# Kernel optimization log

Hardware: AMD Instinct MI355X
Metric: run time of the kernel (lower is better)

The kernel has to match this reference:

```python
import jax, jax.numpy as jnp
import numpy as np
import math

H = 5       # attention heads
DK = 20     # attdim // H
ATT = 100   # attdim
LAYERS = 2
B, L, BERT_DIM = 32, 256, 768


def _layernorm(x, a, b, eps=1e-6):
    mean = x.mean(-1, keepdims=True)
    std = jnp.std(x, axis=-1, ddof=1, keepdims=True)  # torch.std is unbiased
    return a * (x - mean) / (std + eps) + b


def _forward(sequence_output, src_mask, aspect_mask, short_mask,
             ln_a, ln_b, Wxx_w, Wxx_b, q_w, q_b, k_w, k_b,
             dense_w, dense_b, bias_m, W_w, W_b, Wx_w, Wx_b, clf_w, clf_b):
    Bn, Ln, _ = sequence_output.shape
    x = _layernorm(sequence_output, ln_a, ln_b)
    g = x @ Wxx_w + Wxx_b                                  # [B,L,100]
    asp_wn = aspect_mask.sum(1, keepdims=True)             # [B,1]
    aspect = (g * aspect_mask[..., None]).sum(1) / asp_wn  # [B,100]

    q = (g @ q_w + q_b).reshape(Bn, Ln, H, DK).transpose(0, 2, 1, 3)  # [B,H,L,dk]
    k = (g @ k_w + k_b).reshape(Bn, Ln, H, DK).transpose(0, 2, 1, 3)
    # aspect is expanded identically across heads/positions before dense -> [B,dk]
    asp = aspect @ dense_w + dense_b                       # [B,dk]
    scores = jnp.einsum('bhid,bhjd->bhij', q, k) / math.sqrt(DK)
    asp_sc = jnp.tanh(jnp.einsum('bd,bhjd->bhj', asp, k) + bias_m[0])
    scores = scores + asp_sc[:, :, None, :]
    scores = jnp.where(src_mask[:, None, None, :] == 0, -1e9, scores)
    scores = scores + short_mask                           # [B,1,L,L] broadcast
    adj = jax.nn.softmax(scores, axis=-1)                  # [B,H,L,L]

    # edge-update linear split so the [B,L,L,205] concat is never materialized:
    # edge[b,i,j] = adj_perm[b,i,j] @ Wa + go[b,j] @ W1 + go[b,i] @ W2 + b
    Wa, W1, W2 = Wx_w[:H], Wx_w[H:H + ATT], Wx_w[H + ATT:]
    go = g
    for i in range(LAYERS):
        # expand+matmul+mean over heads == mean-head message passing
        Ax = jnp.einsum('bhij,bjd->bid', adj, go) / H
        go = jax.nn.relu(Ax @ W_w + W_b)
        if i < LAYERS - 1:  # last edge update is discarded by the original output
            edge = (jnp.einsum('bhij,hk->bijk', adj, Wa)
                    + (go @ W1)[:, None, :, :]
                    + (go @ W2)[:, :, None, :]
                    + Wx_b)
            adj = edge.transpose(0, 3, 1, 2)
    # original: node_outputs = F.relu(gcn_outputs) (aggregate_W result is overwritten)
    h = jax.nn.relu(go)
    out1 = (h * aspect_mask[..., None]).sum(1) / asp_wn    # [B,100]
    return out1 @ clf_w + clf_b                            # [B,3]


def setup_inputs() -> dict:
    key = jax.random.key(0)
    ks = jax.random.split(key, 24)
    f32 = jnp.float32
    p = lambda k, shape, s=0.05: jax.random.normal(k, shape, dtype=f32) * s
    src_mask = jax.random.randint(ks[0], (B, L), 0, 2, dtype=jnp.int32).at[:, 0].set(1)
    aspect_mask = jnp.zeros((B, L), f32).at[:, 4:8].set(1.0)  # aspect span tokens
    return {
        'sequence_output': jax.random.normal(ks[1], (B, L, BERT_DIM), dtype=f32),
        'src_mask': src_mask,
        'aspect_mask': aspect_mask,
        'short_mask': p(ks[2], (B, 1, L, L), 1.0),
        'ln_a': jnp.ones((BERT_DIM,), f32),
        'ln_b': jnp.zeros((BERT_DIM,), f32),
        'Wxx_w': p(ks[3], (BERT_DIM, ATT)), 'Wxx_b': p(ks[4], (ATT,)),
        'q_w': p(ks[5], (ATT, ATT)), 'q_b': p(ks[6], (ATT,)),
        'k_w': p(ks[7], (ATT, ATT)), 'k_b': p(ks[8], (ATT,)),
        'dense_w': p(ks[9], (ATT, DK)), 'dense_b': p(ks[10], (DK,)),
        'bias_m': p(ks[11], (1,)),
        'W_w': p(ks[12], (ATT, ATT)), 'W_b': p(ks[13], (ATT,)),
        'Wx_w': p(ks[14], (H + 2 * ATT, H)), 'Wx_b': p(ks[15], (H,)),
        'clf_w': p(ks[16], (ATT, 3)), 'clf_b': p(ks[17], (3,)),
    }


def reference(sequence_output, src_mask, aspect_mask, short_mask,
              ln_a, ln_b, Wxx_w, Wxx_b, q_w, q_b, k_w, k_b,
              dense_w, dense_b, bias_m, W_w, W_b, Wx_w, Wx_b, clf_w, clf_b):
    return _forward(sequence_output, src_mask, aspect_mask, short_mask,
                    ln_a, ln_b, Wxx_w, Wxx_b, q_w, q_b, k_w, k_b,
                    dense_w, dense_b, bias_m, W_w, W_b, Wx_w, Wx_b, clf_w, clf_b)
```

## Files before the change

kernel.cpp:

```cpp
#include <hip/hip_runtime.h>
#include <math.h>

constexpr int CL = 256;
constexpr int CD = 768;
constexpr int CATT = 100;
constexpr int CH = 5;
constexpr int CDK = 20;
constexpr unsigned NBLK = 512;

__device__ __forceinline__ void fma4(float4& a, float s, const float4& w) {
    a.x = fmaf(s, w.x, a.x);
    a.y = fmaf(s, w.y, a.y);
    a.z = fmaf(s, w.z, a.z);
    a.w = fmaf(s, w.w, a.w);
}

__device__ __forceinline__ void bbar(unsigned* ctr, unsigned target, bool poll) {
    __syncthreads();
    if (threadIdx.x == 0) {
        __hip_atomic_fetch_add(ctr, 1u, __ATOMIC_RELEASE, __HIP_MEMORY_SCOPE_AGENT);
        if (poll) {
            while (__hip_atomic_load(ctr, __ATOMIC_RELAXED, __HIP_MEMORY_SCOPE_AGENT) < target) {
                __builtin_amdgcn_s_sleep(2);
            }
        }
    }
    __syncthreads();
    __builtin_amdgcn_fence(__ATOMIC_ACQUIRE, "agent");
}

__global__ __launch_bounds__(256, 2) void fused_all(
    const float* __restrict__ x, const int* __restrict__ src_mask,
    const float* __restrict__ amask, const float* __restrict__ shortm,
    const float* __restrict__ ln_a, const float* __restrict__ ln_b,
    const float* __restrict__ Wxx_w, const float* __restrict__ Wxx_b,
    const float* __restrict__ q_w, const float* __restrict__ q_b,
    const float* __restrict__ k_w, const float* __restrict__ k_b,
    const float* __restrict__ dense_w, const float* __restrict__ dense_b,
    const float* __restrict__ bias_m, const float* __restrict__ W_w,
    const float* __restrict__ W_b, const float* __restrict__ Wx_w,
    const float* __restrict__ Wx_b, const float* __restrict__ clf_w,
    const float* __restrict__ clf_b,
    float* __restrict__ g, float* __restrict__ ktb,
    float* __restrict__ go1, float* __restrict__ aspect_raw,
    float* __restrict__ t1, float* __restrict__ t2,
    float* __restrict__ out1_raw, unsigned* __restrict__ bar,
    float* __restrict__ out)
{
    __shared__ __align__(16) float S[12744];

    const int t = threadIdx.x;
    const int lane = t & 63, wid = t >> 6;
    const int blk = blockIdx.x;
    const int xcd = blk & 7;
    const int slot = blk >> 3;
    const int batch = xcd * 4 + (slot >> 4);
    const int icb = slot & 15;
    unsigned* bctr = bar + batch * 32;

    {
        float* s_wB   = S + 4160;
        float* s_xn   = S + 0;
        float* s_gt   = S + 1152;
        float* s_ln   = S + 10560;
        float* s_qq   = S + 10560;
        float* s_mean = S + 12160;
        float* s_rinv = S + 12176;
        const int r0 = batch * 256 + icb * 16;

        if (t < 192) {
            ((float4*)s_ln)[t] = ((const float4*)ln_a)[t];
            ((float4*)(s_ln + 768))[t] = ((const float4*)ln_b)[t];
        }

        for (int rr = wid * 4; rr < wid * 4 + 4; ++rr) {
            const float* xr = x + (size_t)(r0 + rr) * CD;
            float xv[12];
            float s = 0.f;
#pragma unroll
            for (int m = 0; m < 12; ++m) { xv[m] = xr[lane + 64 * m]; s += xv[m]; }
#pragma unroll
            for (int o = 32; o; o >>= 1) s += __shfl_xor(s, o);
            float mean = s * (1.0f / 768.0f);
            float sq = 0.f;
#pragma unroll
            for (int m = 0; m < 12; ++m) { float d = xv[m] - mean; sq = fmaf(d, d, sq); }
#pragma unroll
            for (int o = 32; o; o >>= 1) sq += __shfl_xor(sq, o);
            if (lane == 0) {
                s_mean[rr] = mean;
                s_rinv[rr] = 1.0f / (sqrtf(sq * (1.0f / 767.0f)) + 1e-6f);
            }
        }

        const float4* wsrc = (const float4*)Wxx_w;
        float4 w0 = wsrc[t], w1 = wsrc[t + 256], w2 = wsrc[t + 512], w3;
        if (t < 32) w3 = wsrc[t + 768];
        const int rA = t >> 5, cA = t & 31;
        float xa = x[(size_t)(r0 + rA) * CD + cA];
        float xb = x[(size_t)(r0 + rA + 8) * CD + cA];

        __syncthreads();

        {
            float4* d4 = (float4*)s_wB;
            d4[t] = w0; d4[t + 256] = w1; d4[t + 512] = w2;
            if (t < 32) d4[t + 768] = w3;
            float la = s_ln[cA], lbv = s_ln[768 + cA];
            s_xn[rA * 36 + cA] = fmaf(la, (xa - s_mean[rA]) * s_rinv[rA], lbv);
            s_xn[(rA + 8) * 36 + cA] = fmaf(la, (xb - s_mean[rA + 8]) * s_rinv[rA + 8], lbv);
        }
        __syncthreads();

        const int cgi = t % 25, rg = t / 25;
        const int c = cgi * 4;
        float4 acc0 = make_float4(0.f, 0.f, 0.f, 0.f);
        float4 acc1 = make_float4(0.f, 0.f, 0.f, 0.f);

        for (int kt = 0; kt < 24; ++kt) {
            if (kt < 23) {
                const float4* ws = wsrc + (size_t)(kt + 1) * 800;
                w0 = ws[t]; w1 = ws[t + 256]; w2 = ws[t + 512];
                if (t < 32) w3 = ws[t + 768];
                int gc = (kt + 1) * 32 + cA;
                xa = x[(size_t)(r0 + rA) * CD + gc];
                xb = x[(size_t)(r0 + rA + 8) * CD + gc];
            }
            if (t < 200) {
                const float* wb = s_wB + (kt & 1) * 3200;
                const float* xbuf = s_xn + (kt & 1) * 576;
#pragma unroll 2
                for (int kk = 0; kk < 32; kk += 4) {
                    float4 a0 = *(const float4*)&xbuf[(rg * 2 + 0) * 36 + kk];
                    float4 a1 = *(const float4*)&xbuf[(rg * 2 + 1) * 36 + kk];
                    float4 v0 = *(const float4*)&wb[(kk + 0) * 100 + c];
                    float4 v1 = *(const float4*)&wb[(kk + 1) * 100 + c];
                    float4 v2 = *(const float4*)&wb[(kk + 2) * 100 + c];
                    float4 v3 = *(const float4*)&wb[(kk + 3) * 100 + c];
                    fma4(acc0, a0.x, v0); fma4(acc0, a0.y, v1); fma4(acc0, a0.z, v2); fma4(acc0, a0.w, v3);
                    fma4(acc1, a1.x, v0); fma4(acc1, a1.y, v1); fma4(acc1, a1.z, v2); fma4(acc1, a1.w, v3);
                }
            }
            if (kt < 23) {
                float4* d4 = (float4*)(s_wB + ((kt + 1) & 1) * 3200);
                d4[t] = w0; d4[t + 256] = w1; d4[t + 512] = w2;
                if (t < 32) d4[t + 768] = w3;
                int gc = (kt + 1) * 32 + cA;
                float la = s_ln[gc], lbv = s_ln[768 + gc];
                float* xd = s_xn + ((kt + 1) & 1) * 576;
                xd[rA * 36 + cA] = fmaf(la, (xa - s_mean[rA]) * s_rinv[rA], lbv);
                xd[(rA + 8) * 36 + cA] = fmaf(la, (xb - s_mean[rA + 8]) * s_rinv[rA + 8], lbv);
            }
            __syncthreads();
        }

        if (t < 200) {
            float4 bias = *(const float4*)&Wxx_b[c];
            float4 rv0, rv1;
            rv0.x = acc0.x + bias.x; rv0.y = acc0.y + bias.y; rv0.z = acc0.z + bias.z; rv0.w = acc0.w + bias.w;
            rv1.x = acc1.x + bias.x; rv1.y = acc1.y + bias.y; rv1.z = acc1.z + bias.z; rv1.w = acc1.w + bias.w;
            float4 rv[2] = { rv0, rv1 };
#pragma unroll
            for (int q = 0; q < 2; ++q) {
                int row = r0 + rg * 2 + q;
                *(float4*)&g[(size_t)row * CATT + c] = rv[q];
                *(float4*)&s_gt[(rg * 2 + q) * 100 + c] = rv[q];
                float m = amask[row];
                if (m != 0.f) {
                    atomicAdd(&aspect_raw[batch * CATT + c + 0], m * rv[q].x);
                    atomicAdd(&aspect_raw[batch * CATT + c + 1], m * rv[q].y);
                    atomicAdd(&aspect_raw[batch * CATT + c + 2], m * rv[q].z);
                    atomicAdd(&aspect_raw[batch * CATT + c + 3], m * rv[q].w);
                }
            }
        }

        const float4* qw4 = (const float4*)q_w;
        const float4* kw4 = (const float4*)k_w;
        float4 sA = qw4[t], sB;
        if (t < 244) sB = qw4[t + 256];
        __syncthreads();
        {
            float4* d4 = (float4*)s_wB;
            d4[t] = sA; if (t < 244) d4[t + 256] = sB;
        }
        __syncthreads();

        float4 p0 = make_float4(0.f, 0.f, 0.f, 0.f);
        float4 p1 = make_float4(0.f, 0.f, 0.f, 0.f);
        for (int tau = 0; tau < 10; ++tau) {
            if (tau < 9) {
                const float4* src = (tau + 1 < 5) ? qw4 + (size_t)(tau + 1) * 500
                                                  : kw4 + (size_t)(tau - 4) * 500;
                sA = src[t]; if (t < 244) sB = src[t + 256];
            }
            if (t < 200) {
                const float* wb = s_wB + (tau & 1) * 3200;
                const int kb = (tau % 5) * 20;
#pragma unroll 2
                for (int kk = 0; kk < 20; kk += 4) {
                    float4 a0 = *(const float4*)&s_gt[(rg * 2 + 0) * 100 + kb + kk];
                    float4 a1 = *(const float4*)&s_gt[(rg * 2 + 1) * 100 + kb + kk];
                    float4 v0 = *(const float4*)&wb[(kk + 0) * 100 + c];
                    float4 v1 = *(const float4*)&wb[(kk + 1) * 100 + c];
                    float4 v2 = *(const float4*)&wb[(kk + 2) * 100 + c];
                    float4 v3 = *(const float4*)&wb[(kk + 3) * 100 + c];
                    fma4(p0, a0.x, v0); fma4(p0, a0.y, v1); fma4(p0, a0.z, v2); fma4(p0, a0.w, v3);
                    fma4(p1, a1.x, v0); fma4(p1, a1.y, v1); fma4(p1, a1.z, v2); fma4(p1, a1.w, v3);
                }
                if (tau == 4 || tau == 9) {
                    const float* bb = (tau == 4) ? q_b : k_b;
                    float4 bias = *(const float4*)&bb[c];
                    p0.x += bias.x; p0.y += bias.y; p0.z += bias.z; p0.w += bias.w;
                    p1.x += bias.x; p1.y += bias.y; p1.z += bias.z; p1.w += bias.w;
                    const int h = c / CDK, d = c % CDK;
                    if (tau == 4) {
                        *(float4*)&s_qq[h * 320 + (rg * 2 + 0) * CDK + d] = p0;
                        *(float4*)&s_qq[h * 320 + (rg * 2 + 1) * CDK + d] = p1;
                    } else {
                        float4 rv[2] = { p0, p1 };
#pragma unroll
                        for (int q = 0; q < 2; ++q) {
                            int row = r0 + rg * 2 + q;
                            int l = row & 255;
                            *(float4*)&ktb[((size_t)(batch * CH + h) * CL + l) * CDK + d] = rv[q];
                        }
                    }
                    p0 = make_float4(0.f, 0.f, 0.f, 0.f);
                    p1 = make_float4(0.f, 0.f, 0.f, 0.f);
                }
            }
            if (tau < 9) {
                float4* d4 = (float4*)(s_wB + ((tau + 1) & 1) * 3200);
                d4[t] = sA; if (t < 244) d4[t + 256] = sB;
            }
            __syncthreads();
        }
    }

    bbar(bctr, 16, true);

    {
        constexpr int ICH = 16;
        float* s_pool  = S + 0;
        float* s_wB    = S + 4160;
        float* s_q     = S + 10560;
        float* s_red   = S + 12160;
        float* s_was   = S + 12480;
        float* s_aspb  = S + 12488;
        float* s_w1    = S + 12512;
        float* s_w2    = S + 12612;
        float* s_g1row = S + 12712;
        float* s_gw2   = S + 12728;

        const int b = batch, i0 = icb * ICH;
        const int j = t;

        if (t < 5) {
            float s = 0.f;
            for (int k2 = 0; k2 < 5; ++k2) s += Wx_w[t * 5 + k2];
            s_was[t] = s;
        }
        if (t < 100) {
            float a = 0.f, c2 = 0.f;
#pragma unroll
            for (int h = 0; h < 5; ++h) {
                a += Wx_w[(5 + t) * 5 + h];
                c2 += Wx_w[(105 + t) * 5 + h];
            }
            s_w1[t] = a; s_w2[t] = c2;
        }
        float wn = 0.f;
        if (t < 64) {
            float4 mv = ((const float4*)amask)[b * 64 + t];
            wn = mv.x + mv.y + mv.z + mv.w;
#pragma unroll
            for (int o = 32; o; o >>= 1) wn += __shfl_xor(wn, o);
        }
        if (t < 20) {
            float a = 0.f;
            for (int d = 0; d < CATT; ++d)
                a = fmaf(aspect_raw[b * CATT + d], dense_w[d * CDK + t], a);
            s_aspb[t] = a / wn + dense_b[t];
        }

        const bool masked = (src_mask[b * CL + j] == 0);
        const float bm = bias_m[0];
        const float rs20 = 0.223606797749978969f;

        float sm[ICH];
#pragma unroll
        for (int ii = 0; ii < ICH; ++ii)
            sm[ii] = shortm[(size_t)(b * CL + i0 + ii) * CL + j];

        float accS[ICH], accW[ICH];
#pragma unroll
        for (int ii = 0; ii < ICH; ++ii) { accS[ii] = 0.f; accW[ii] = 0.f; }

        __syncthreads();

        for (int h = 0; h < CH; ++h) {
            float4 kr[5];
            const float* kp = ktb + ((size_t)(b * CH + h) * CL + j) * CDK;
#pragma unroll
            for (int m = 0; m < 5; ++m) kr[m] = *(const float4*)(kp + 4 * m);
            const float was_h = s_was[h];
            float s = bm;
#pragma unroll
            for (int m = 0; m < 5; ++m) {
                s = fmaf(s_aspb[4 * m + 0], kr[m].x, s);
                s = fmaf(s_aspb[4 * m + 1], kr[m].y, s);
                s = fmaf(s_aspb[4 * m + 2], kr[m].z, s);
                s = fmaf(s_aspb[4 * m + 3], kr[m].w, s);
            }
            const float aspsc = tanhf(s);

            float pv[ICH];
#pragma unroll
            for (int ii = 0; ii < ICH; ++ii) {
                const float* qrow = &s_q[h * 320 + ii * CDK];
                float sc = 0.f;
#pragma unroll
                for (int m = 0; m < 5; ++m) {
                    float4 q4 = *(const float4*)(qrow + 4 * m);
                    sc = fmaf(q4.x, kr[m].x, sc);
                    sc = fmaf(q4.y, kr[m].y, sc);
                    sc = fmaf(q4.z, kr[m].z, sc);
                    sc = fmaf(q4.w, kr[m].w, sc);
                }
                sc = fmaf(sc, rs20, aspsc) + sm[ii];
                float p = masked ? 0.f : __expf(sc);
                pv[ii] = p;
                float ssum = p;
#pragma unroll
                for (int o = 32; o; o >>= 1) ssum += __shfl_xor(ssum, o);
                if (lane == 0) s_red[h * 64 + ii * 4 + wid] = ssum;
            }
            __syncthreads();
#pragma unroll
            for (int ii = 0; ii < ICH; ++ii) {
                float tot = s_red[h * 64 + ii * 4 + 0] + s_red[h * 64 + ii * 4 + 1] +
                            s_red[h * 64 + ii * 4 + 2] + s_red[h * 64 + ii * 4 + 3];
                float pn = pv[ii] * __frcp_rn(tot);
                accS[ii] += pn;
                accW[ii] = fmaf(was_h, pn, accW[ii]);
            }
        }

#pragma unroll
        for (int ii = 0; ii < ICH; ++ii)
            s_pool[ii * 260 + j] = accS[ii];

        const int cgi = t % 25, rg = t / 25;
        const int c = cgi * 4;
        const float4* g4 = (const float4*)g + (size_t)b * 6400;
        float4 sA = g4[t], sB = g4[t + 256], sC = g4[t + 512], sD;
        if (t < 32) sD = g4[t + 768];
        {
            float4* d4 = (float4*)s_wB;
            d4[t] = sA; d4[t + 256] = sB; d4[t + 512] = sC;
            if (t < 32) d4[t + 768] = sD;
        }
        __syncthreads();

        float4 acc0 = make_float4(0.f, 0.f, 0.f, 0.f);
        float4 acc1 = make_float4(0.f, 0.f, 0.f, 0.f);
        for (int jt = 0; jt < 8; ++jt) {
            if (jt < 7) {
                const float4* src = g4 + (size_t)(jt + 1) * 800;
                sA = src[t]; sB = src[t + 256]; sC = src[t + 512];
                if (t < 32) sD = src[t + 768];
            }
            if (t < 200) {
                const float* wb = s_wB + (jt & 1) * 3200;
#pragma unroll 2
                for (int kk = 0; kk < 32; kk += 4) {
                    float4 a0 = *(const float4*)&s_pool[(rg * 2 + 0) * 260 + jt * 32 + kk];
                    float4 a1 = *(const float4*)&s_pool[(rg * 2 + 1) * 260 + jt * 32 + kk];
                    float4 v0 = *(const float4*)&wb[(kk + 0) * 100 + c];
                    float4 v1 = *(const float4*)&wb[(kk + 1) * 100 + c];
                    float4 v2 = *(const float4*)&wb[(kk + 2) * 100 + c];
                    float4 v3 = *(const float4*)&wb[(kk + 3) * 100 + c];
                    fma4(acc0, a0.x, v0); fma4(acc0, a0.y, v1); fma4(acc0, a0.z, v2); fma4(acc0, a0.w, v3);
                    fma4(acc1, a1.x, v0); fma4(acc1, a1.y, v1); fma4(acc1, a1.z, v2); fma4(acc1, a1.w, v3);
                }
            }
            if (jt < 7) {
                float4* d4 = (float4*)(s_wB + ((jt + 1) & 1) * 3200);
                d4[t] = sA; d4[t + 256] = sB; d4[t + 512] = sC;
                if (t < 32) d4[t + 768] = sD;
            }
            __syncthreads();
        }

        float* s_ax = s_pool;
        if (t < 200) {
            float4 r;
            r.x = acc0.x * 0.2f; r.y = acc0.y * 0.2f; r.z = acc0.z * 0.2f; r.w = acc0.w * 0.2f;
            *(float4*)&s_ax[(rg * 2 + 0) * 108 + c] = r;
            r.x = acc1.x * 0.2f; r.y = acc1.y * 0.2f; r.z = acc1.z * 0.2f; r.w = acc1.w * 0.2f;
            *(float4*)&s_ax[(rg * 2 + 1) * 108 + c] = r;
        }
        const float4* ww4 = (const float4*)W_w;
        sA = ww4[t]; if (t < 244) sB = ww4[t + 256];
        {
            float4* d4 = (float4*)s_wB;
            d4[t] = sA; if (t < 244) d4[t + 256] = sB;
        }
        __syncthreads();

        float4 o0 = make_float4(0.f, 0.f, 0.f, 0.f);
        float4 o1 = make_float4(0.f, 0.f, 0.f, 0.f);
        for (int wt = 0; wt < 5; ++wt) {
            if (wt < 4) {
                const float4* src = ww4 + (size_t)(wt + 1) * 500;
                sA = src[t]; if (t < 244) sB = src[t + 256];
            }
            if (t < 200) {
                const float* wb = s_wB + (wt & 1) * 3200;
                const int kb = wt * 20;
#pragma unroll 2
                for (int kk = 0; kk < 20; kk += 4) {
                    float4 a0 = *(const float4*)&s_ax[(rg * 2 + 0) * 108 + kb + kk];
                    float4 a1 = *(const float4*)&s_ax[(rg * 2 + 1) * 108 + kb + kk];
                    float4 v0 = *(const float4*)&wb[(kk + 0) * 100 + c];
                    float4 v1 = *(const float4*)&wb[(kk + 1) * 100 + c];
                    float4 v2 = *(const float4*)&wb[(kk + 2) * 100 + c];
                    float4 v3 = *(const float4*)&wb[(kk + 3) * 100 + c];
                    fma4(o0, a0.x, v0); fma4(o0, a0.y, v1); fma4(o0, a0.z, v2); fma4(o0, a0.w, v3);
                    fma4(o1, a1.x, v0); fma4(o1, a1.y, v1); fma4(o1, a1.z, v2); fma4(o1, a1.w, v3);
                }
            }
            if (wt < 4) {
                float4* d4 = (float4*)(s_wB + ((wt + 1) & 1) * 3200);
                d4[t] = sA; if (t < 244) d4[t + 256] = sB;
            }
            __syncthreads();
        }

        float* s_go = s_pool + 1728;
        if (t < 200) {
            float4 bias = *(const float4*)&W_b[c];
            o0.x = fmaxf(o0.x + bias.x, 0.f); o0.y = fmaxf(o0.y + bias.y, 0.f);
            o0.z = fmaxf(o0.z + bias.z, 0.f); o0.w = fmaxf(o0.w + bias.w, 0.f);
            o1.x = fmaxf(o1.x + bias.x, 0.f); o1.y = fmaxf(o1.y + bias.y, 0.f);
            o1.z = fmaxf(o1.z + bias.z, 0.f); o1.w = fmaxf(o1.w + bias.w, 0.f);
            *(float4*)&go1[(size_t)(b * CL + i0 + rg * 2 + 0) * CATT + c] = o0;
            *(float4*)&go1[(size_t)(b * CL + i0 + rg * 2 + 1) * CATT + c] = o1;
            *(float4*)&s_go[(rg * 2 + 0) * 104 + c] = o0;
            *(float4*)&s_go[(rg * 2 + 1) * 104 + c] = o1;
        }
        __syncthreads();

        if (t < 128) {
            int r = t >> 3, seg = t & 7;
            int e0 = seg * 13, e1 = e0 + 13 < 100 ? e0 + 13 : 100;
            float a = 0.f, c2 = 0.f;
            for (int e = e0; e < e1; ++e) {
                float v = s_go[r * 104 + e];
                a = fmaf(v, s_w1[e], a);
                c2 = fmaf(v, s_w2[e], c2);
            }
            a += __shfl_xor(a, 1); a += __shfl_xor(a, 2); a += __shfl_xor(a, 4);
            c2 += __shfl_xor(c2, 1); c2 += __shfl_xor(c2, 2); c2 += __shfl_xor(c2, 4);
            if (seg == 0) {
                s_g1row[r] = a;
                s_gw2[r] = c2;
            }
        }
        __syncthreads();

        if (t < 100) {
            float a = 0.f, s2 = 0.f;
#pragma unroll
            for (int r = 0; r < 16; ++r) {
                float v = s_go[r * 104 + t];
                a = fmaf(s_g1row[r], v, a);
                s2 += v;
            }
            atomicAdd(&t1[b * CATT + t], a);
            atomicAdd(&t2[b * CATT + t], s2);
        }
        __syncthreads();

#pragma unroll
        for (int ii = 0; ii < ICH; ++ii)
            s_pool[ii * 260 + j] = accW[ii];
    }

    bbar(bctr, 32, true);

    {
        float* s_pool = S + 0;
        float* s_wB   = S + 4160;
        float* s_gw2  = S + 12728;

        const int b = batch, i0 = icb * 16;
        const int cgi = t % 25, rg = t / 25;
        const int c = cgi * 4;

        const float4* g4 = (const float4*)go1 + (size_t)b * 6400;
        float4 sA = g4[t], sB = g4[t + 256], sC = g4[t + 512], sD;
        if (t < 32) sD = g4[t + 768];
        {
            float4* d4 = (float4*)s_wB;
            d4[t] = sA; d4[t + 256] = sB; d4[t + 512] = sC;
            if (t < 32) d4[t + 768] = sD;
        }
        __syncthreads();

        float4 acc0 = make_float4(0.f, 0.f, 0.f, 0.f);
        float4 acc1 = make_float4(0.f, 0.f, 0.f, 0.f);
        for (int jt = 0; jt < 8; ++jt) {
            if (jt < 7) {
                const float4* src = g4 + (size_t)(jt + 1) * 800;
                sA = src[t]; sB = src[t + 256]; sC = src[t + 512];
                if (t < 32) sD = src[t + 768];
            }
            if (t < 200) {
                const float* wb = s_wB + (jt & 1) * 3200;
#pragma unroll 2
                for (int kk = 0; kk < 32; kk += 4) {
                    float4 a0 = *(const float4*)&s_pool[(rg * 2 + 0) * 260 + jt * 32 + kk];
                    float4 a1 = *(const float4*)&s_pool[(rg * 2 + 1) * 260 + jt * 32 + kk];
                    float4 v0 = *(const float4*)&wb[(kk + 0) * 100 + c];
                    float4 v1 = *(const float4*)&wb[(kk + 1) * 100 + c];
                    float4 v2 = *(const float4*)&wb[(kk + 2) * 100 + c];
                    float4 v3 = *(const float4*)&wb[(kk + 3) * 100 + c];
                    fma4(acc0, a0.x, v0); fma4(acc0, a0.y, v1); fma4(acc0, a0.z, v2); fma4(acc0, a0.w, v3);
                    fma4(acc1, a1.x, v0); fma4(acc1, a1.y, v1); fma4(acc1, a1.z, v2); fma4(acc1, a1.w, v3);
                }
            }
            if (jt < 7) {
                float4* d4 = (float4*)(s_wB + ((jt + 1) & 1) * 3200);
                d4[t] = sA; d4[t + 256] = sB; d4[t + 512] = sC;
                if (t < 32) d4[t + 768] = sD;
            }
            __syncthreads();
        }

        float* s_ax = s_pool;
        if (t < 200) {
            float wxbs = Wx_b[0] + Wx_b[1] + Wx_b[2] + Wx_b[3] + Wx_b[4];
            float4 t1v = *(const float4*)&t1[b * CATT + c];
            float4 t2v = *(const float4*)&t2[b * CATT + c];
            float gw0 = s_gw2[rg * 2 + 0] + wxbs;
            float gw1 = s_gw2[rg * 2 + 1] + wxbs;
            float4 r;
            r.x = (acc0.x + t1v.x + gw0 * t2v.x) * 0.2f;
            r.y = (acc0.y + t1v.y + gw0 * t2v.y) * 0.2f;
            r.z = (acc0.z + t1v.z + gw0 * t2v.z) * 0.2f;
            r.w = (acc0.w + t1v.w + gw0 * t2v.w) * 0.2f;
            *(float4*)&s_ax[(rg * 2 + 0) * 108 + c] = r;
            r.x = (acc1.x + t1v.x + gw1 * t2v.x) * 0.2f;
            r.y = (acc1.y + t1v.y + gw1 * t2v.y) * 0.2f;
            r.z = (acc1.z + t1v.z + gw1 * t2v.z) * 0.2f;
            r.w = (acc1.w + t1v.w + gw1 * t2v.w) * 0.2f;
            *(float4*)&s_ax[(rg * 2 + 1) * 108 + c] = r;
        }
        const float4* ww4 = (const float4*)W_w;
        sA = ww4[t]; if (t < 244) sB = ww4[t + 256];
        {
            float4* d4 = (float4*)s_wB;
            d4[t] = sA; if (t < 244) d4[t + 256] = sB;
        }
        __syncthreads();

        float4 o0 = make_float4(0.f, 0.f, 0.f, 0.f);
        float4 o1 = make_float4(0.f, 0.f, 0.f, 0.f);
        for (int wt = 0; wt < 5; ++wt) {
            if (wt < 4) {
                const float4* src = ww4 + (size_t)(wt + 1) * 500;
                sA = src[t]; if (t < 244) sB = src[t + 256];
            }
            if (t < 200) {
                const float* wb = s_wB + (wt & 1) * 3200;
                const int kb = wt * 20;
#pragma unroll 2
                for (int kk = 0; kk < 20; kk += 4) {
                    float4 a0 = *(const float4*)&s_ax[(rg * 2 + 0) * 108 + kb + kk];
                    float4 a1 = *(const float4*)&s_ax[(rg * 2 + 1) * 108 + kb + kk];
                    float4 v0 = *(const float4*)&wb[(kk + 0) * 100 + c];
                    float4 v1 = *(const float4*)&wb[(kk + 1) * 100 + c];
                    float4 v2 = *(const float4*)&wb[(kk + 2) * 100 + c];
                    float4 v3 = *(const float4*)&wb[(kk + 3) * 100 + c];
                    fma4(o0, a0.x, v0); fma4(o0, a0.y, v1); fma4(o0, a0.z, v2); fma4(o0, a0.w, v3);
                    fma4(o1, a1.x, v0); fma4(o1, a1.y, v1); fma4(o1, a1.z, v2); fma4(o1, a1.w, v3);
                }
            }
            if (wt < 4) {
                float4* d4 = (float4*)(s_wB + ((wt + 1) & 1) * 3200);
                d4[t] = sA; if (t < 244) d4[t + 256] = sB;
            }
            __syncthreads();
        }

        if (t < 200) {
            float4 bias = *(const float4*)&W_b[c];
            o0.x = fmaxf(o0.x + bias.x, 0.f); o0.y = fmaxf(o0.y + bias.y, 0.f);
            o0.z = fmaxf(o0.z + bias.z, 0.f); o0.w = fmaxf(o0.w + bias.w, 0.f);
            o1.x = fmaxf(o1.x + bias.x, 0.f); o1.y = fmaxf(o1.y + bias.y, 0.f);
            o1.z = fmaxf(o1.z + bias.z, 0.f); o1.w = fmaxf(o1.w + bias.w, 0.f);
            float4 ov[2] = { o0, o1 };
#pragma unroll
            for (int q = 0; q < 2; ++q) {
                int row = b * CL + i0 + rg * 2 + q;
                float m = amask[row];
                if (m != 0.f) {
                    atomicAdd(&out1_raw[b * CATT + c + 0], m * ov[q].x);
                    atomicAdd(&out1_raw[b * CATT + c + 1], m * ov[q].y);
                    atomicAdd(&out1_raw[b * CATT + c + 2], m * ov[q].z);
                    atomicAdd(&out1_raw[b * CATT + c + 3], m * ov[q].w);
                }
            }
        }
    }

    bbar(bctr, 48, icb == 0);

    if (icb == 0 && t < 64) {
        const int b = batch;
        float4 mv = ((const float4*)amask)[b * 64 + t];
        float wn = mv.x + mv.y + mv.z + mv.w;
#pragma unroll
        for (int o = 32; o; o >>= 1) wn += __shfl_xor(wn, o);
        if (t < 3) {
            float rwn = 1.f / wn;
            float a = clf_b[t];
            for (int d = 0; d < CATT; ++d)
                a = fmaf(out1_raw[b * CATT + d] * rwn, clf_w[d * 3 + t], a);
            out[b * 3 + t] = a;
        }
    }
}

extern "C" void kernel_launch(void* const* d_in, const int* in_sizes, int n_in,
                              void* d_out, int out_size, void* d_ws, size_t ws_size,
                              hipStream_t stream) {
    const float* seq     = (const float*)d_in[0];
    const int*   srcm    = (const int*)d_in[1];
    const float* amask   = (const float*)d_in[2];
    const float* shortm  = (const float*)d_in[3];
    const float* ln_a    = (const float*)d_in[4];
    const float* ln_b    = (const float*)d_in[5];
    const float* Wxx_w   = (const float*)d_in[6];
    const float* Wxx_b   = (const float*)d_in[7];
    const float* q_w     = (const float*)d_in[8];
    const float* q_b     = (const float*)d_in[9];
    const float* k_w     = (const float*)d_in[10];
    const float* k_b     = (const float*)d_in[11];
    const float* dense_w = (const float*)d_in[12];
    const float* dense_b = (const float*)d_in[13];
    const float* bias_m  = (const float*)d_in[14];
    const float* W_w     = (const float*)d_in[15];
    const float* W_b     = (const float*)d_in[16];
    const float* Wx_w    = (const float*)d_in[17];
    const float* Wx_b    = (const float*)d_in[18];
    const float* clf_w   = (const float*)d_in[19];
    const float* clf_b   = (const float*)d_in[20];
    float* out = (float*)d_out;

    float* ws         = (float*)d_ws;
    float* g          = ws;
    float* ktb        = g + 819200;
    float* go1        = ktb + 819200;
    float* aspect_raw = go1 + 819200;
    float* t1         = aspect_raw + 3200;
    float* t2         = t1 + 3200;
    float* out1_raw   = t2 + 3200;
    unsigned* bar     = (unsigned*)(out1_raw + 3200);

    hipMemsetAsync(aspect_raw, 0, 4 * 3200 * sizeof(float) + 32 * 32 * sizeof(unsigned), stream);

    hipLaunchKernelGGL(fused_all, dim3(NBLK), dim3(256), 0, stream,
                       seq, srcm, amask, shortm, ln_a, ln_b, Wxx_w, Wxx_b,
                       q_w, q_b, k_w, k_b, dense_w, dense_b, bias_m,
                       W_w, W_b, Wx_w, Wx_b, clf_w, clf_b,
                       g, ktb, go1, aspect_raw, t1, t2, out1_raw, bar, out);
}
```

Baseline: 283.6 us.

## Hoist short-mask loads, prefetch next-head K, reorder Q/K projection, fully unroll inner loops

The short_mask rows are loaded into registers at kernel start, so their latency overlaps the first phase instead of stalling after the grid barrier. The per-head K loads in the attention loop are software-pipelined by prefetching the next head's K vector. The Q/K projection order is swapped so K (needed by other blocks via global memory) is written first, and the inner FMA loops are fully unrolled. This raises register pressure (16 mask floats live across phases plus prefetch registers), which may cut occupancy under launch_bounds(256,2).

Result: slower. 302.0 us (+6.5%).

```diff
diff --git a/kernel.cpp b/kernel.cpp
--- a/kernel.cpp
+++ b/kernel.cpp
@@ -47,6 +47,7 @@
     float* __restrict__ out1_raw, unsigned* __restrict__ bar,
     float* __restrict__ out)
 {
+    constexpr int ICH = 16;
     __shared__ __align__(16) float S[12744];
 
     const int t = threadIdx.x;
@@ -57,6 +58,11 @@
     const int batch = xcd * 4 + (slot >> 4);
     const int icb = slot & 15;
     unsigned* bctr = bar + batch * 32;
+
+    float sm[ICH];
+#pragma unroll
+    for (int ii = 0; ii < ICH; ++ii)
+        sm[ii] = shortm[(size_t)(batch * CL + icb * ICH + ii) * CL + t];
 
     {
         float* s_wB   = S + 4160;
@@ -129,7 +135,7 @@
             if (t < 200) {
                 const float* wb = s_wB + (kt & 1) * 3200;
                 const float* xbuf = s_xn + (kt & 1) * 576;
-#pragma unroll 2
+#pragma unroll
                 for (int kk = 0; kk < 32; kk += 4) {
                     float4 a0 = *(const float4*)&xbuf[(rg * 2 + 0) * 36 + kk];
                     float4 a1 = *(const float4*)&xbuf[(rg * 2 + 1) * 36 + kk];
@@ -177,8 +183,8 @@
 
         const float4* qw4 = (const float4*)q_w;
         const float4* kw4 = (const float4*)k_w;
-        float4 sA = qw4[t], sB;
-        if (t < 244) sB = qw4[t + 256];
+        float4 sA = kw4[t], sB;
+        if (t < 244) sB = kw4[t + 256];
         __syncthreads();
         {
             float4* d4 = (float4*)s_wB;
@@ -190,14 +196,14 @@
         float4 p1 = make_float4(0.f, 0.f, 0.f, 0.f);
         for (int tau = 0; tau < 10; ++tau) {
             if (tau < 9) {
-                const float4* src = (tau + 1 < 5) ? qw4 + (size_t)(tau + 1) * 500
-                                                  : kw4 + (size_t)(tau - 4) * 500;
+                const float4* src = (tau + 1 < 5) ? kw4 + (size_t)(tau + 1) * 500
+                                                  : qw4 + (size_t)(tau - 4) * 500;
                 sA = src[t]; if (t < 244) sB = src[t + 256];
             }
             if (t < 200) {
                 const float* wb = s_wB + (tau & 1) * 3200;
                 const int kb = (tau % 5) * 20;
-#pragma unroll 2
+#pragma unroll
                 for (int kk = 0; kk < 20; kk += 4) {
                     float4 a0 = *(const float4*)&s_gt[(rg * 2 + 0) * 100 + kb + kk];
                     float4 a1 = *(const float4*)&s_gt[(rg * 2 + 1) * 100 + kb + kk];
@@ -209,15 +215,12 @@
                     fma4(p1, a1.x, v0); fma4(p1, a1.y, v1); fma4(p1, a1.z, v2); fma4(p1, a1.w, v3);
                 }
                 if (tau == 4 || tau == 9) {
-                    const float* bb = (tau == 4) ? q_b : k_b;
+                    const float* bb = (tau == 4) ? k_b : q_b;
                     float4 bias = *(const float4*)&bb[c];
                     p0.x += bias.x; p0.y += bias.y; p0.z += bias.z; p0.w += bias.w;
                     p1.x += bias.x; p1.y += bias.y; p1.z += bias.z; p1.w += bias.w;
                     const int h = c / CDK, d = c % CDK;
                     if (tau == 4) {
-                        *(float4*)&s_qq[h * 320 + (rg * 2 + 0) * CDK + d] = p0;
-                        *(float4*)&s_qq[h * 320 + (rg * 2 + 1) * CDK + d] = p1;
-                    } else {
                         float4 rv[2] = { p0, p1 };
 #pragma unroll
                         for (int q = 0; q < 2; ++q) {
@@ -225,6 +228,9 @@
                             int l = row & 255;
                             *(float4*)&ktb[((size_t)(batch * CH + h) * CL + l) * CDK + d] = rv[q];
                         }
+                    } else {
+                        *(float4*)&s_qq[h * 320 + (rg * 2 + 0) * CDK + d] = p0;
+                        *(float4*)&s_qq[h * 320 + (rg * 2 + 1) * CDK + d] = p1;
                     }
                     p0 = make_float4(0.f, 0.f, 0.f, 0.f);
                     p1 = make_float4(0.f, 0.f, 0.f, 0.f);
@@ -241,7 +247,6 @@
     bbar(bctr, 16, true);
 
     {
-        constexpr int ICH = 16;
         float* s_pool  = S + 0;
         float* s_wB    = S + 4160;
         float* s_q     = S + 10560;
@@ -288,22 +293,25 @@
         const float bm = bias_m[0];
         const float rs20 = 0.223606797749978969f;
 
-        float sm[ICH];
-#pragma unroll
-        for (int ii = 0; ii < ICH; ++ii)
-            sm[ii] = shortm[(size_t)(b * CL + i0 + ii) * CL + j];
-
         float accS[ICH], accW[ICH];
 #pragma unroll
         for (int ii = 0; ii < ICH; ++ii) { accS[ii] = 0.f; accW[ii] = 0.f; }
 
         __syncthreads();
 
+        const float* kbase = ktb + (size_t)(b * CH) * CL * CDK + (size_t)j * CDK;
+        float4 kr[5];
+#pragma unroll
+        for (int m = 0; m < 5; ++m) kr[m] = *(const float4*)(kbase + 4 * m);
+
+#pragma unroll
         for (int h = 0; h < CH; ++h) {
-            float4 kr[5];
-            const float* kp = ktb + ((size_t)(b * CH + h) * CL + j) * CDK;
-#pragma unroll
-            for (int m = 0; m < 5; ++m) kr[m] = *(const float4*)(kp + 4 * m);
+            float4 krn[5];
+            if (h < CH - 1) {
+                const float* kpn = kbase + (size_t)(h + 1) * CL * CDK;
+#pragma unroll
+                for (int m = 0; m < 5; ++m) krn[m] = *(const float4*)(kpn + 4 * m);
+            }
             const float was_h = s_was[h];
             float s = bm;
 #pragma unroll
@@ -344,6 +352,10 @@
                 float pn = pv[ii] * __frcp_rn(tot);
                 accS[ii] += pn;
                 accW[ii] = fmaf(was_h, pn, accW[ii]);
+            }
+            if (h < CH - 1) {
+#pragma unroll
+                for (int m = 0; m < 5; ++m) kr[m] = krn[m];
             }
         }
 
@@ -373,7 +385,7 @@
             }
             if (t < 200) {
                 const float* wb = s_wB + (jt & 1) * 3200;
-#pragma unroll 2
+#pragma unroll
                 for (int kk = 0; kk < 32; kk += 4) {
                     float4 a0 = *(const float4*)&s_pool[(rg * 2 + 0) * 260 + jt * 32 + kk];
                     float4 a1 = *(const float4*)&s_pool[(rg * 2 + 1) * 260 + jt * 32 + kk];
@@ -419,7 +431,7 @@
             if (t < 200) {
                 const float* wb = s_wB + (wt & 1) * 3200;
                 const int kb = wt * 20;
-#pragma unroll 2
+#pragma unroll
                 for (int kk = 0; kk < 20; kk += 4) {
                     float4 a0 = *(const float4*)&s_ax[(rg * 2 + 0) * 108 + kb + kk];
                     float4 a1 = *(const float4*)&s_ax[(rg * 2 + 1) * 108 + kb + kk];
@@ -519,7 +531,7 @@
             }
             if (t < 200) {
                 const float* wb = s_wB + (jt & 1) * 3200;
-#pragma unroll 2
+#pragma unroll
                 for (int kk = 0; kk < 32; kk += 4) {
                     float4 a0 = *(const float4*)&s_pool[(rg * 2 + 0) * 260 + jt * 32 + kk];
                     float4 a1 = *(const float4*)&s_pool[(rg * 2 + 1) * 260 + jt * 32 + kk];
@@ -576,7 +588,7 @@
             if (t < 200) {
                 const float* wb = s_wB + (wt & 1) * 3200;
                 const int kb = wt * 20;
-#pragma unroll 2
+#pragma unroll
                 for (int kk = 0; kk < 20; kk += 4) {
                     float4 a0 = *(const float4*)&s_ax[(rg * 2 + 0) * 108 + kb + kk];
                     float4 a1 = *(const float4*)&s_ax[(rg * 2 + 1) * 108 + kb + kk];
```
